# Optimization experiments

Hardware: AMD Instinct MI355X
Metric: run time of the kernel (lower is better)

## Reference

```python
import jax, jax.numpy as jnp
from jax import lax
import numpy as np

DN = ('NCHW', 'OIHW', 'NCHW')


def _conv(x, w, b):
    y = lax.conv_general_dilated(x, w, (1, 1), 'SAME', dimension_numbers=DN)
    return y + b[None, :, None, None]


def setup_inputs() -> dict:
    key = jax.random.key(0)
    ks = jax.random.split(key, 8)
    B = 2
    noise = 0.1 * jax.random.normal(ks[0], (B, 768, 577), dtype=jnp.float32)  # N(0, 0.1)
    targets = jax.random.randint(ks[1], (B, 384, 384), 0, 171)
    w1 = 0.02 * jax.random.normal(ks[2], (512, 768, 3, 3), dtype=jnp.float32)
    b1 = 0.02 * jax.random.normal(ks[3], (512,), dtype=jnp.float32)
    w2 = 0.02 * jax.random.normal(ks[4], (512, 512, 3, 3), dtype=jnp.float32)
    b2 = 0.02 * jax.random.normal(ks[5], (512,), dtype=jnp.float32)
    w3 = 0.2 * jax.random.normal(ks[6], (77,), dtype=jnp.float32)  # Con3: Conv2d(1,77,1x1)
    b3 = 0.2 * jax.random.normal(ks[7], (77,), dtype=jnp.float32)
    return {'noise': noise, 'targets': targets, 'w1': w1, 'b1': b1,
            'w2': w2, 'b2': b2, 'w3': w3, 'b3': b3}


def reference(noise, targets, w1, b1, w2, b2, w3, b3):
    B = noise.shape[0]
    # NoiseToImage is shadowed by an empty nn.Sequential() -> identity
    image_noise = jnp.transpose(noise, (2, 0, 1))  # (577, B, 768)

    # --- NoiseToText ---
    H, W = targets.shape[1], targets.shape[2]
    ih = (jnp.arange(24) * H) // 24  # nearest-neighbor interpolate indices
    iw = (jnp.arange(24) * W) // 24
    m = targets[:, ih][:, :, iw]  # (B, 24, 24) class labels
    # one-hot scatter into 256 channels, keep first 171 (labels >=171 -> all-zero)
    mask = (m[:, None] == jnp.arange(171)[None, :, None, None]).astype(noise.dtype)  # (B,171,24,24)

    x = noise[:, :, 1:].reshape(B, 768, 24, 24)  # drop CLS token
    xm = x[:, None] * mask[:, :, None]            # (B,171,768,24,24)
    xm = xm.reshape(B * 171, 768, 24, 24)

    y = _conv(xm, w1, b1)                         # (B*171,512,24,24)
    y = y.reshape(-1, 512, 6, 4, 6, 4).mean(axis=(3, 5))  # AdaptiveAvgPool2d((6,6))
    y = _conv(y, w2, b2)                          # (B*171,512,6,6)
    y = y.mean(axis=(2, 3))                       # AdaptiveAvgPool2d((1,1)) -> (B*171,512)
    y = y.reshape(B, 171, 1, 512).transpose(0, 2, 1, 3)  # (B,1,171,512)
    # Con3: 1x1 conv with in_channels=1, out_channels=77
    text_noise = w3[None, :, None, None] * y + b3[None, :, None, None]  # (B,77,171,512)
    return image_noise, text_noise
```

## Files before the change

kernel.cpp:

```cpp
#include <hip/hip_runtime.h>
#include <hip/hip_bf16.h>

typedef unsigned short u16;
typedef short bf16x8 __attribute__((ext_vector_type(8)));
typedef float f32x4 __attribute__((ext_vector_type(4)));

__device__ __forceinline__ u16 f2bf(float f){
    unsigned u = __float_as_uint(f);
    unsigned r = 0x7fffu + ((u >> 16) & 1u);
    return (u16)((u + r) >> 16);
}

__device__ __forceinline__ void gload_lds16(const u16* g, u16* lds_base){
    __builtin_amdgcn_global_load_lds(
        (const __attribute__((address_space(1))) unsigned int*)g,
        (__attribute__((address_space(3))) unsigned int*)lds_base, 16, 0, 0);
}

#define OUT0_N 886272
#define OUT1_N 13483008
#define YN 175104
#define KSPLIT 24

__global__ void k_prep(const float* __restrict__ noise, const int* __restrict__ targets,
                       const float* __restrict__ w1, const float* __restrict__ b1,
                       const float* __restrict__ w2, const float* __restrict__ b2,
                       float* __restrict__ out0, u16* __restrict__ XbfT,
                       u16* __restrict__ Are, float* __restrict__ Mfull,
                       float* __restrict__ bias, int* __restrict__ labels){
    __shared__ float sh[32 * 33];
    int blk = blockIdx.x;
    int tid = threadIdx.x;
    if (blk < 912){
        int b   = blk / 456;
        int rem = blk % 456;
        int cb  = rem / 19, sb = rem % 19;
        int tx = tid & 31, ty = tid >> 5;
        int s0 = sb * 32, c0 = cb * 32;
        float (*tile)[33] = (float(*)[33])sh;
        #pragma unroll
        for (int i = 0; i < 4; i++){
            int c = c0 + ty + i * 8;
            int s = s0 + tx;
            if (s < 577) tile[ty + i * 8][tx] = noise[(size_t)(b * 768 + c) * 577 + s];
        }
        __syncthreads();
        #pragma unroll
        for (int i = 0; i < 4; i++){
            int s = s0 + ty + i * 8;
            int c = c0 + tx;
            if (s >= 577) continue;
            float v = tile[tx][ty + i * 8];
            out0[(size_t)(s * 2 + b) * 768 + c] = v;
            if (s >= 1) XbfT[(size_t)(b * 576 + s - 1) * 768 + c] = f2bf(v);
        }
    } else if (blk < 2448){
        int idx = (blk - 912) * 256 + tid;
        int k = idx % 768; int c1 = idx / 768;
        const float* wp = w1 + (size_t)idx * 9;
        #pragma unroll
        for (int tap = 0; tap < 9; tap++)
            Are[(size_t)(c1 * 9 + tap) * 768 + k] = f2bf(wp[tap]);
    } else if (blk < 3472){
        int idx = (blk - 2448) * 256 + tid;
        int c1 = idx % 512, c2 = idx / 512;
        const float* wp = w2 + (size_t)(c2 * 512 + c1) * 9;
        float t[3][3];
        #pragma unroll
        for (int r = 0; r < 3; r++)
            #pragma unroll
            for (int s = 0; s < 3; s++)
                t[r][s] = wp[r * 3 + s];
        float cs0[3], cs1[3], cs2[3];
        #pragma unroll
        for (int r = 0; r < 3; r++){
            cs0[r] = t[r][0] + t[r][1];
            cs1[r] = t[r][0] + t[r][1] + t[r][2];
            cs2[r] = t[r][1] + t[r][2];
        }
        const float inv = 1.0f / 576.0f;
        float* Mp = Mfull + (size_t)(c2 * 512 + c1) * 9;
        Mp[0] = inv * (cs0[0] + cs0[1]);
        Mp[1] = inv * (cs1[0] + cs1[1]);
        Mp[2] = inv * (cs2[0] + cs2[1]);
        Mp[3] = inv * (cs0[0] + cs0[1] + cs0[2]);
        Mp[4] = inv * (cs1[0] + cs1[1] + cs1[2]);
        Mp[5] = inv * (cs2[0] + cs2[1] + cs2[2]);
        Mp[6] = inv * (cs0[1] + cs0[2]);
        Mp[7] = inv * (cs1[1] + cs1[2]);
        Mp[8] = inv * (cs2[1] + cs2[2]);
    } else if (blk < 3984){
        int c2 = blk - 3472;
        const float cw[9] = {25.f,30.f,25.f,30.f,36.f,30.f,25.f,30.f,25.f};
        float sb = 0.f;
        for (int c1 = tid; c1 < 512; c1 += 256){
            const float* wp = w2 + (size_t)(c2 * 512 + c1) * 9;
            float s = 0.f;
            #pragma unroll
            for (int q = 0; q < 9; q++) s += wp[q] * cw[q];
            sb += b1[c1] * s;
        }
        sh[tid] = sb; __syncthreads();
        for (int o = 128; o > 0; o >>= 1){ if (tid < o) sh[tid] += sh[tid + o]; __syncthreads(); }
        if (tid == 0) bias[c2] = b2[c2] + sh[0] * (1.0f / 36.0f);
    } else {
        int idx = (blk - 3984) * 256 + tid;
        if (idx < 1152){
            int b = idx / 576; int p = idx % 576;
            int i = p / 24, j = p % 24;
            labels[idx] = targets[b * 147456 + i * 16 * 384 + j * 16];
        }
    }
}

__launch_bounds__(256)
__global__ void k_gemm1(const u16* __restrict__ Are, const u16* __restrict__ XbfT,
                        float* __restrict__ D){
    __shared__ u16 As[128 * 64];
    __shared__ u16 Bs[64 * 64];
    int tid  = threadIdx.x;
    int wave = tid >> 6, lane = tid & 63;
    int l16 = lane & 15, quad = lane >> 4;
    int wm = wave >> 1, wn = wave & 1;
    int m0 = blockIdx.x * 128;
    int n0 = blockIdx.y * 64;
    int srow = lane >> 3, scol = (lane & 7) * 8;
    f32x4 acc[4][2] = {};
    for (int k0 = 0; k0 < 768; k0 += 64){
        #pragma unroll
        for (int j = 0; j < 4; j++){
            int ch = wave * 4 + j;
            gload_lds16(Are + (size_t)(m0 + ch * 8 + srow) * 768 + k0 + scol, &As[ch * 512]);
        }
        #pragma unroll
        for (int j = 0; j < 2; j++){
            int ch = wave * 2 + j;
            gload_lds16(XbfT + (size_t)(n0 + ch * 8 + srow) * 768 + k0 + scol, &Bs[ch * 512]);
        }
        __syncthreads();
        #pragma unroll
        for (int ks = 0; ks < 2; ks++){
            bf16x8 af[4], bf[2];
            #pragma unroll
            for (int i = 0; i < 4; i++)
                af[i] = *(const bf16x8*)&As[(wm * 64 + i * 16 + l16) * 64 + ks * 32 + quad * 8];
            #pragma unroll
            for (int i = 0; i < 2; i++)
                bf[i] = *(const bf16x8*)&Bs[(wn * 32 + i * 16 + l16) * 64 + ks * 32 + quad * 8];
            #pragma unroll
            for (int mi = 0; mi < 4; mi++)
                #pragma unroll
                for (int ni = 0; ni < 2; ni++)
                    acc[mi][ni] = __builtin_amdgcn_mfma_f32_16x16x32_bf16(af[mi], bf[ni], acc[mi][ni], 0, 0, 0);
        }
        __syncthreads();
    }
    #pragma unroll
    for (int mi = 0; mi < 4; mi++)
        #pragma unroll
        for (int ni = 0; ni < 2; ni++)
            #pragma unroll
            for (int r = 0; r < 4; r++)
                D[(size_t)(m0 + wm * 64 + mi * 16 + quad * 4 + r) * 1152 + n0 + wn * 32 + ni * 16 + l16] = acc[mi][ni][r];
}

__launch_bounds__(256)
__global__ void k_scatter(const float* __restrict__ D, const int* __restrict__ labels,
                          float* __restrict__ Zcat){
    int blk = blockIdx.x;
    int b  = blk >> 9;
    int c1 = blk & 511;
    __shared__ float acc[171 * 9];
    int t = threadIdx.x;
    for (int q = t; q < 1539; q += 256) acc[q] = 0.f;
    __syncthreads();
    for (int p = t; p < 576; p += 256){
        int cls = labels[b * 576 + p];
        if (cls < 0 || cls >= 171) continue;
        int i = p / 24, j = p % 24;
        float slot[9];
        #pragma unroll
        for (int q = 0; q < 9; q++) slot[q] = 0.f;
        unsigned used = 0;
        int tau[3]; bool vs[3];
        #pragma unroll
        for (int s1 = 0; s1 < 3; s1++){
            int v = j - s1 + 1;
            vs[s1]  = (v >= 0 && v < 24);
            tau[s1] = (v < 4) ? 0 : ((v < 20) ? 1 : 2);
        }
        #pragma unroll
        for (int r1 = 0; r1 < 3; r1++){
            int u = i - r1 + 1;
            if (u < 0 || u >= 24) continue;
            int rho = (u < 4) ? 0 : ((u < 20) ? 1 : 2);
            #pragma unroll
            for (int s1 = 0; s1 < 3; s1++){
                if (!vs[s1]) continue;
                float tv = D[(size_t)(c1 * 9 + r1 * 3 + s1) * 1152 + b * 576 + p];
                int sl = rho * 3 + tau[s1];
                slot[sl] += tv;
                used |= 1u << sl;
            }
        }
        #pragma unroll
        for (int sl = 0; sl < 9; sl++)
            if (used & (1u << sl)) atomicAdd(&acc[cls * 9 + sl], slot[sl]);
    }
    __syncthreads();
    for (int q = t; q < 1539; q += 256){
        int cls = q / 9, sl = q % 9;
        Zcat[(size_t)(b * 171 + cls) * 4608 + c1 * 9 + sl] = acc[q];
    }
}

__launch_bounds__(256)
__global__ void k_gemm2p(const float* __restrict__ Mfull, const float* __restrict__ Zcat,
                         float* __restrict__ ypart){
    __shared__ __align__(16) float As[16][68];
    __shared__ __align__(16) float Bs[16][68];
    int m0 = blockIdx.x * 64;
    int n0 = blockIdx.y * 64;
    int s  = blockIdx.z;
    int kbeg = s * 192;
    int t  = threadIdx.x;
    int tx = t % 16, ty = t / 16;
    float acc[4][4] = {};
    for (int k0 = kbeg; k0 < kbeg + 192; k0 += 16){
        #pragma unroll
        for (int e = t; e < 1024; e += 256){
            int r = e / 16, c = e % 16;
            As[c][r] = Mfull[(size_t)(m0 + r) * 4608 + k0 + c];
        }
        #pragma unroll
        for (int e = t; e < 1024; e += 256){
            int r = e / 16, c = e % 16;
            int n = n0 + r;
            Bs[c][r] = (n < 342) ? Zcat[(size_t)n * 4608 + k0 + c] : 0.f;
        }
        __syncthreads();
        #pragma unroll
        for (int kk = 0; kk < 16; kk++){
            float4 a4 = *(const float4*)&As[kk][ty * 4];
            float4 b4 = *(const float4*)&Bs[kk][tx * 4];
            float a[4] = {a4.x, a4.y, a4.z, a4.w};
            float bb[4] = {b4.x, b4.y, b4.z, b4.w};
            #pragma unroll
            for (int mi = 0; mi < 4; mi++)
                #pragma unroll
                for (int ni = 0; ni < 4; ni++)
                    acc[mi][ni] += a[mi] * bb[ni];
        }
        __syncthreads();
    }
    float* yp = ypart + (size_t)s * YN;
    #pragma unroll
    for (int ni = 0; ni < 4; ni++){
        int n = n0 + tx * 4 + ni;
        if (n >= 342) continue;
        float4 v = make_float4(acc[0][ni], acc[1][ni], acc[2][ni], acc[3][ni]);
        *(float4*)&yp[(size_t)n * 512 + m0 + ty * 4] = v;
    }
}

__global__ void k_gemm2r(const float* __restrict__ ypart, const float* __restrict__ bias,
                         float* __restrict__ y){
    int idx = blockIdx.x * 256 + threadIdx.x;
    if (idx >= YN) return;
    float sum = bias[idx & 511];
    #pragma unroll 4
    for (int s = 0; s < KSPLIT; s++) sum += ypart[(size_t)s * YN + idx];
    y[idx] = sum;
}

__global__ void k_final(const float* __restrict__ y, const float* __restrict__ w3,
                        const float* __restrict__ b3, float4* __restrict__ out1){
    int idx = blockIdx.x * 256 + threadIdx.x;
    if (idx >= OUT1_N / 4) return;
    int c4 = idx & 127;
    int r = idx >> 7;
    int cls = r % 171; r /= 171;
    int o = r % 77;
    int b = r / 77;
    float4 v = *(const float4*)&y[(size_t)(b * 171 + cls) * 512 + c4 * 4];
    float w = w3[o], bb = b3[o];
    out1[idx] = make_float4(w * v.x + bb, w * v.y + bb, w * v.z + bb, w * v.w + bb);
}

extern "C" void kernel_launch(void* const* d_in, const int* in_sizes, int n_in,
                              void* d_out, int out_size, void* d_ws, size_t ws_size,
                              hipStream_t stream) {
    const float* noise   = (const float*)d_in[0];
    const int*   targets = (const int*)  d_in[1];
    const float* w1      = (const float*)d_in[2];
    const float* b1      = (const float*)d_in[3];
    const float* w2      = (const float*)d_in[4];
    const float* b2      = (const float*)d_in[5];
    const float* w3      = (const float*)d_in[6];
    const float* b3      = (const float*)d_in[7];
    float* out0 = (float*)d_out;
    float* out1 = out0 + OUT0_N;

    char* ws = (char*)d_ws;
    const size_t OFF_ARE  = 0;
    const size_t OFF_X    = 7077888;
    const size_t OFF_D    = OFF_X   + 1769472;
    const size_t OFF_MF   = OFF_D   + 21233664;
    const size_t OFF_ZC   = OFF_MF  + 9437184;
    const size_t OFF_Y    = OFF_ZC  + 6303744;
    const size_t OFF_BIAS = OFF_Y   + 700416;
    const size_t OFF_LAB  = OFF_BIAS + 2048;

    u16*   Are   = (u16*)  (ws + OFF_ARE);
    u16*   XbfT  = (u16*)  (ws + OFF_X);
    float* D     = (float*)(ws + OFF_D);
    float* ypart = (float*)(ws + OFF_D);
    float* Mfull = (float*)(ws + OFF_MF);
    float* Zcat  = (float*)(ws + OFF_ZC);
    float* yb    = (float*)(ws + OFF_Y);
    float* bias  = (float*)(ws + OFF_BIAS);
    int*   labels= (int*)  (ws + OFF_LAB);

    k_prep  <<<3989, 256, 0, stream>>>(noise, targets, w1, b1, w2, b2,
                                       out0, XbfT, Are, Mfull, bias, labels);
    k_gemm1 <<<dim3(36, 18), 256, 0, stream>>>(Are, XbfT, D);
    k_scatter<<<1024, 256, 0, stream>>>(D, labels, Zcat);
    k_gemm2p<<<dim3(8, 6, KSPLIT), 256, 0, stream>>>(Mfull, Zcat, ypart);
    k_gemm2r<<<(YN + 255) / 256, 256, 0, stream>>>(ypart, bias, yb);
    k_final <<<(OUT1_N / 4 + 255) / 256, 256, 0, stream>>>(yb, w3, b3, (float4*)out1);
}
```

Before: 189.7 us.

## Run second conv GEMM on bf16 MFMA and fuse reduction with output broadcast

Stores the pooled conv2 weight matrix and the scattered class features as bf16 and replaces the fp32 SIMT split-K GEMM with an MFMA bf16 GEMM using direct global-to-LDS loads. Padding rows of the feature matrix are zeroed in the prep kernel so no bounds checks are needed in the GEMM. The split-K reduction, bias add and the 77-way Con3 broadcast are merged into one kernel, which removes the intermediate y buffer and one launch. This trades precision for throughput, and the fused final kernel runs only 171 blocks that each write 77 strided outputs.

```diff
diff --git a/kernel.cpp b/kernel.cpp
--- a/kernel.cpp
+++ b/kernel.cpp
@@ -20,14 +20,15 @@
 #define OUT0_N 886272
 #define OUT1_N 13483008
 #define YN 175104
-#define KSPLIT 24
+#define KS2 24
 
 __global__ void k_prep(const float* __restrict__ noise, const int* __restrict__ targets,
                        const float* __restrict__ w1, const float* __restrict__ b1,
                        const float* __restrict__ w2, const float* __restrict__ b2,
                        float* __restrict__ out0, u16* __restrict__ XbfT,
-                       u16* __restrict__ Are, float* __restrict__ Mfull,
-                       float* __restrict__ bias, int* __restrict__ labels){
+                       u16* __restrict__ Are, u16* __restrict__ Mfull16,
+                       float* __restrict__ bias, int* __restrict__ labels,
+                       u16* __restrict__ Zcat16){
     __shared__ float sh[32 * 33];
     int blk = blockIdx.x;
     int tid = threadIdx.x;
@@ -79,16 +80,16 @@
             cs2[r] = t[r][1] + t[r][2];
         }
         const float inv = 1.0f / 576.0f;
-        float* Mp = Mfull + (size_t)(c2 * 512 + c1) * 9;
-        Mp[0] = inv * (cs0[0] + cs0[1]);
-        Mp[1] = inv * (cs1[0] + cs1[1]);
-        Mp[2] = inv * (cs2[0] + cs2[1]);
-        Mp[3] = inv * (cs0[0] + cs0[1] + cs0[2]);
-        Mp[4] = inv * (cs1[0] + cs1[1] + cs1[2]);
-        Mp[5] = inv * (cs2[0] + cs2[1] + cs2[2]);
-        Mp[6] = inv * (cs0[1] + cs0[2]);
-        Mp[7] = inv * (cs1[1] + cs1[2]);
-        Mp[8] = inv * (cs2[1] + cs2[2]);
+        u16* Mp = Mfull16 + (size_t)(c2 * 512 + c1) * 9;
+        Mp[0] = f2bf(inv * (cs0[0] + cs0[1]));
+        Mp[1] = f2bf(inv * (cs1[0] + cs1[1]));
+        Mp[2] = f2bf(inv * (cs2[0] + cs2[1]));
+        Mp[3] = f2bf(inv * (cs0[0] + cs0[1] + cs0[2]));
+        Mp[4] = f2bf(inv * (cs1[0] + cs1[1] + cs1[2]));
+        Mp[5] = f2bf(inv * (cs2[0] + cs2[1] + cs2[2]));
+        Mp[6] = f2bf(inv * (cs0[1] + cs0[2]));
+        Mp[7] = f2bf(inv * (cs1[1] + cs1[2]));
+        Mp[8] = f2bf(inv * (cs2[1] + cs2[2]));
     } else if (blk < 3984){
         int c2 = blk - 3472;
         const float cw[9] = {25.f,30.f,25.f,30.f,36.f,30.f,25.f,30.f,25.f};
@@ -103,13 +104,16 @@
         sh[tid] = sb; __syncthreads();
         for (int o = 128; o > 0; o >>= 1){ if (tid < o) sh[tid] += sh[tid + o]; __syncthreads(); }
         if (tid == 0) bias[c2] = b2[c2] + sh[0] * (1.0f / 36.0f);
-    } else {
+    } else if (blk < 3989){
         int idx = (blk - 3984) * 256 + tid;
         if (idx < 1152){
             int b = idx / 576; int p = idx % 576;
             int i = p / 24, j = p % 24;
             labels[idx] = targets[b * 147456 + i * 16 * 384 + j * 16];
         }
+    } else {
+        int idx = (blk - 3989) * 256 + tid;
+        if (idx < 193536) Zcat16[342 * 4608 + idx] = 0;
     }
 }
 
@@ -166,7 +170,7 @@
 
 __launch_bounds__(256)
 __global__ void k_scatter(const float* __restrict__ D, const int* __restrict__ labels,
-                          float* __restrict__ Zcat){
+                          u16* __restrict__ Zcat16){
     int blk = blockIdx.x;
     int b  = blk >> 9;
     int c1 = blk & 511;
@@ -210,81 +214,92 @@
     __syncthreads();
     for (int q = t; q < 1539; q += 256){
         int cls = q / 9, sl = q % 9;
-        Zcat[(size_t)(b * 171 + cls) * 4608 + c1 * 9 + sl] = acc[q];
+        Zcat16[(size_t)(b * 171 + cls) * 4608 + c1 * 9 + sl] = f2bf(acc[q]);
     }
 }
 
 __launch_bounds__(256)
-__global__ void k_gemm2p(const float* __restrict__ Mfull, const float* __restrict__ Zcat,
+__global__ void k_gemm2m(const u16* __restrict__ Zcat16, const u16* __restrict__ Mfull16,
                          float* __restrict__ ypart){
-    __shared__ __align__(16) float As[16][68];
-    __shared__ __align__(16) float Bs[16][68];
-    int m0 = blockIdx.x * 64;
+    __shared__ u16 As[128 * 64];
+    __shared__ u16 Bs[64 * 64];
+    int tid  = threadIdx.x;
+    int wave = tid >> 6, lane = tid & 63;
+    int l16 = lane & 15, quad = lane >> 4;
+    int wm = wave >> 1, wn = wave & 1;
+    int m0 = blockIdx.x * 128;
     int n0 = blockIdx.y * 64;
-    int s  = blockIdx.z;
-    int kbeg = s * 192;
-    int t  = threadIdx.x;
-    int tx = t % 16, ty = t / 16;
-    float acc[4][4] = {};
-    for (int k0 = kbeg; k0 < kbeg + 192; k0 += 16){
-        #pragma unroll
-        for (int e = t; e < 1024; e += 256){
-            int r = e / 16, c = e % 16;
-            As[c][r] = Mfull[(size_t)(m0 + r) * 4608 + k0 + c];
-        }
-        #pragma unroll
-        for (int e = t; e < 1024; e += 256){
-            int r = e / 16, c = e % 16;
-            int n = n0 + r;
-            Bs[c][r] = (n < 342) ? Zcat[(size_t)n * 4608 + k0 + c] : 0.f;
-        }
-        __syncthreads();
-        #pragma unroll
-        for (int kk = 0; kk < 16; kk++){
-            float4 a4 = *(const float4*)&As[kk][ty * 4];
-            float4 b4 = *(const float4*)&Bs[kk][tx * 4];
-            float a[4] = {a4.x, a4.y, a4.z, a4.w};
-            float bb[4] = {b4.x, b4.y, b4.z, b4.w};
+    int kbeg = blockIdx.z * 192;
+    int srow = lane >> 3, scol = (lane & 7) * 8;
+    f32x4 acc[4][2] = {};
+    for (int k0 = kbeg; k0 < kbeg + 192; k0 += 64){
+        #pragma unroll
+        for (int j = 0; j < 4; j++){
+            int ch = wave * 4 + j;
+            gload_lds16(Zcat16 + (size_t)(m0 + ch * 8 + srow) * 4608 + k0 + scol, &As[ch * 512]);
+        }
+        #pragma unroll
+        for (int j = 0; j < 2; j++){
+            int ch = wave * 2 + j;
+            gload_lds16(Mfull16 + (size_t)(n0 + ch * 8 + srow) * 4608 + k0 + scol, &Bs[ch * 512]);
+        }
+        __syncthreads();
+        #pragma unroll
+        for (int ks = 0; ks < 2; ks++){
+            bf16x8 af[4], bf[2];
+            #pragma unroll
+            for (int i = 0; i < 4; i++)
+                af[i] = *(const bf16x8*)&As[(wm * 64 + i * 16 + l16) * 64 + ks * 32 + quad * 8];
+            #pragma unroll
+            for (int i = 0; i < 2; i++)
+                bf[i] = *(const bf16x8*)&Bs[(wn * 32 + i * 16 + l16) * 64 + ks * 32 + quad * 8];
             #pragma unroll
             for (int mi = 0; mi < 4; mi++)
                 #pragma unroll
-                for (int ni = 0; ni < 4; ni++)
-                    acc[mi][ni] += a[mi] * bb[ni];
-        }
-        __syncthreads();
-    }
-    float* yp = ypart + (size_t)s * YN;
+                for (int ni = 0; ni < 2; ni++)
+                    acc[mi][ni] = __builtin_amdgcn_mfma_f32_16x16x32_bf16(af[mi], bf[ni], acc[mi][ni], 0, 0, 0);
+        }
+        __syncthreads();
+    }
+    float* yp = ypart + (size_t)blockIdx.z * YN;
     #pragma unroll
-    for (int ni = 0; ni < 4; ni++){
-        int n = n0 + tx * 4 + ni;
-        if (n >= 342) continue;
-        float4 v = make_float4(acc[0][ni], acc[1][ni], acc[2][ni], acc[3][ni]);
-        *(float4*)&yp[(size_t)n * 512 + m0 + ty * 4] = v;
-    }
-}
-
-__global__ void k_gemm2r(const float* __restrict__ ypart, const float* __restrict__ bias,
-                         float* __restrict__ y){
-    int idx = blockIdx.x * 256 + threadIdx.x;
-    if (idx >= YN) return;
-    float sum = bias[idx & 511];
+    for (int mi = 0; mi < 4; mi++)
+        #pragma unroll
+        for (int r = 0; r < 4; r++){
+            int n = m0 + wm * 64 + mi * 16 + quad * 4 + r;
+            if (n >= 342) continue;
+            #pragma unroll
+            for (int ni = 0; ni < 2; ni++)
+                yp[(size_t)n * 512 + n0 + wn * 32 + ni * 16 + l16] = acc[mi][ni][r];
+        }
+}
+
+__global__ void k_finalr(const float* __restrict__ ypart, const float* __restrict__ bias,
+                         const float* __restrict__ w3, const float* __restrict__ b3,
+                         float4* __restrict__ out1){
+    __shared__ float w3s[77], b3s[77];
+    int tid = threadIdx.x;
+    if (tid < 77){ w3s[tid] = w3[tid]; b3s[tid] = b3[tid]; }
+    __syncthreads();
+    int idx = blockIdx.x * 256 + tid;
+    if (idx >= YN / 4) return;
+    int c4 = idx & 127;
+    int n  = idx >> 7;
+    const float4* bp = (const float4*)bias;
+    float4 sum = bp[c4];
     #pragma unroll 4
-    for (int s = 0; s < KSPLIT; s++) sum += ypart[(size_t)s * YN + idx];
-    y[idx] = sum;
-}
-
-__global__ void k_final(const float* __restrict__ y, const float* __restrict__ w3,
-                        const float* __restrict__ b3, float4* __restrict__ out1){
-    int idx = blockIdx.x * 256 + threadIdx.x;
-    if (idx >= OUT1_N / 4) return;
-    int c4 = idx & 127;
-    int r = idx >> 7;
-    int cls = r % 171; r /= 171;
-    int o = r % 77;
-    int b = r / 77;
-    float4 v = *(const float4*)&y[(size_t)(b * 171 + cls) * 512 + c4 * 4];
-    float w = w3[o], bb = b3[o];
-    out1[idx] = make_float4(w * v.x + bb, w * v.y + bb, w * v.z + bb, w * v.w + bb);
+    for (int s = 0; s < KS2; s++){
+        float4 v = *(const float4*)&ypart[(size_t)s * YN + (size_t)n * 512 + c4 * 4];
+        sum.x += v.x; sum.y += v.y; sum.z += v.z; sum.w += v.w;
+    }
+    int b = n / 171, cls = n % 171;
+    size_t base = ((size_t)b * 77 * 171 + cls) * 128 + c4;
+    #pragma unroll
+    for (int o = 0; o < 77; o++){
+        float w = w3s[o], bb = b3s[o];
+        out1[base + (size_t)o * 171 * 128] =
+            make_float4(w * sum.x + bb, w * sum.y + bb, w * sum.z + bb, w * sum.w + bb);
+    }
 }
 
 extern "C" void kernel_launch(void* const* d_in, const int* in_sizes, int n_in,
@@ -306,26 +321,23 @@
     const size_t OFF_X    = 7077888;
     const size_t OFF_D    = OFF_X   + 1769472;
     const size_t OFF_MF   = OFF_D   + 21233664;
-    const size_t OFF_ZC   = OFF_MF  + 9437184;
-    const size_t OFF_Y    = OFF_ZC  + 6303744;
-    const size_t OFF_BIAS = OFF_Y   + 700416;
+    const size_t OFF_ZC   = OFF_MF  + 4718592;
+    const size_t OFF_BIAS = OFF_ZC  + 3538944;
     const size_t OFF_LAB  = OFF_BIAS + 2048;
 
-    u16*   Are   = (u16*)  (ws + OFF_ARE);
-    u16*   XbfT  = (u16*)  (ws + OFF_X);
-    float* D     = (float*)(ws + OFF_D);
-    float* ypart = (float*)(ws + OFF_D);
-    float* Mfull = (float*)(ws + OFF_MF);
-    float* Zcat  = (float*)(ws + OFF_ZC);
-    float* yb    = (float*)(ws + OFF_Y);
-    float* bias  = (float*)(ws + OFF_BIAS);
-    int*   labels= (int*)  (ws + OFF_LAB);
-
-    k_prep  <<<3989, 256, 0, stream>>>(noise, targets, w1, b1, w2, b2,
-                                       out0, XbfT, Are, Mfull, bias, labels);
+    u16*   Are    = (u16*)  (ws + OFF_ARE);
+    u16*   XbfT   = (u16*)  (ws + OFF_X);
+    float* D      = (float*)(ws + OFF_D);
+    float* ypart  = (float*)(ws + OFF_D);
+    u16*   Mfull16= (u16*)  (ws + OFF_MF);
+    u16*   Zcat16 = (u16*)  (ws + OFF_ZC);
+    float* bias   = (float*)(ws + OFF_BIAS);
+    int*   labels = (int*)  (ws + OFF_LAB);
+
+    k_prep  <<<4745, 256, 0, stream>>>(noise, targets, w1, b1, w2, b2,
+                                       out0, XbfT, Are, Mfull16, bias, labels, Zcat16);
     k_gemm1 <<<dim3(36, 18), 256, 0, stream>>>(Are, XbfT, D);
-    k_scatter<<<1024, 256, 0, stream>>>(D, labels, Zcat);
-    k_gemm2p<<<dim3(8, 6, KSPLIT), 256, 0, stream>>>(Mfull, Zcat, ypart);
-    k_gemm2r<<<(YN + 255) / 256, 256, 0, stream>>>(ypart, bias, yb);
-    k_final <<<(OUT1_N / 4 + 255) / 256, 256, 0, stream>>>(yb, w3, b3, (float4*)out1);
-}
+    k_scatter<<<1024, 256, 0, stream>>>(D, labels, Zcat16);
+    k_gemm2m<<<dim3(3, 8, KS2), 256, 0, stream>>>(Zcat16, Mfull16, ypart);
+    k_finalr<<<171, 256, 0, stream>>>(ypart, bias, w3, b3, (float4*)out1);
+}
```

New measurement: 158.7 us. 16.3% less time.
